# Kernel optimization log

Measured on AMD Instinct MI355X. Metric: run time of the kernel, lower is better.

Reference implementation:

```python
import jax, jax.numpy as jnp
import numpy as np

NIN = 1024
NOUT = 1024
NHEADS = 16
DHEAD = NOUT // NHEADS


def setup_inputs() -> dict:
    key = jax.random.key(0)
    k1, k2, k3, k4 = jax.random.split(key, 4)
    y = jax.random.normal(k1, (2, 2048, NIN), dtype=jnp.float32)
    Wqkv = jax.random.normal(k2, (NIN, 3 * NOUT), dtype=jnp.float32) * (1.0 / np.sqrt(NIN))
    Wff = jax.random.normal(k3, (NOUT, NOUT), dtype=jnp.float32) * (1.0 / np.sqrt(NOUT))
    bff = jax.random.normal(k4, (NOUT,), dtype=jnp.float32) * 0.01
    return {"y": y, "Wqkv": Wqkv, "Wff": Wff, "bff": bff}


def reference(y, Wqkv, Wff, bff):
    b, n, _ = y.shape
    qkv = y @ Wqkv  # [b, n, 3*nout]
    qkv = qkv.reshape(b, n, 3, NHEADS, DHEAD).transpose(2, 0, 3, 1, 4)
    q, k, v = qkv[0], qkv[1], qkv[2]  # each [b, h, n, d]
    att = jnp.einsum('bhqd,bhkd->bhqk', q, k)
    causal = jnp.triu(jnp.ones((n, n), dtype=bool), k=1)
    att = jnp.where(causal, -jnp.inf, att)
    att = jax.nn.softmax(att / jnp.sqrt(jnp.float32(DHEAD)), axis=-1)
    ctx = jnp.einsum('bhqk,bhkd->bhqd', att, v)
    ctx = ctx.transpose(0, 2, 1, 3).reshape(b, n, NOUT)
    return ctx @ Wff + bff
```

## Files before the change

kernel.cpp:

```cpp
#include <hip/hip_runtime.h>
#include <stdint.h>

#define NHEADS 16
#define DHEAD 64
#define SEQ 2048
#define BATCH 2
#define NINF 1024
#define NOUTF 1024
#define N3 3072
#define MTOT 4096

typedef unsigned short US;
typedef __attribute__((ext_vector_type(8))) short short8;
typedef __attribute__((ext_vector_type(4))) short short4v;
typedef __attribute__((ext_vector_type(4))) float f32x4;

__device__ inline US f2bf(float f) {
  union { float f; unsigned u; } v; v.f = f;
  unsigned r = v.u + 0x7fffu + ((v.u >> 16) & 1u);
  return (US)(r >> 16);
}

__device__ inline f32x4 mfma16(short8 a, short8 b, f32x4 c) {
  return __builtin_amdgcn_mfma_f32_16x16x32_bf16(a, b, c, 0, 0, 0);
}

__device__ inline f32x4 mfma16k16(short4v a, short4v b, f32x4 c) {
  return __builtin_amdgcn_mfma_f32_16x16x16bf16_1k(a, b, c, 0, 0, 0);
}

__device__ inline void async16(const US* g, US* l) {
  __builtin_amdgcn_global_load_lds(
      (const __attribute__((address_space(1))) unsigned int*)g,
      (__attribute__((address_space(3))) unsigned int*)l, 16, 0, 0);
}

__global__ void k_convert(const float* __restrict__ src, US* __restrict__ dst, int n4) {
  int i = blockIdx.x * blockDim.x + threadIdx.x;
  if (i >= n4) return;
  float4 v = ((const float4*)src)[i];
  ushort4 o;
  o.x = f2bf(v.x); o.y = f2bf(v.y); o.z = f2bf(v.z); o.w = f2bf(v.w);
  ((ushort4*)dst)[i] = o;
}

__global__ void k_wtrans(const float* __restrict__ Wqkv, const float* __restrict__ Wff,
                         US* __restrict__ dq, US* __restrict__ df) {
  __shared__ float tile[32][33];
  int bxi = blockIdx.x;
  const float* src; US* dst; int C;
  if (bxi < 96) { src = Wqkv; dst = dq; C = N3; }
  else          { src = Wff;  dst = df; C = NOUTF; bxi -= 96; }
  int bx = bxi * 32, by = blockIdx.y * 32;
  int tx = threadIdx.x, ty = threadIdx.y;
  for (int i = 0; i < 32; i += 8)
    tile[ty + i][tx] = src[(size_t)(by + ty + i) * C + bx + tx];
  __syncthreads();
  for (int i = 0; i < 32; i += 8)
    dst[(size_t)(bx + ty + i) * 1024 + by + tx] = f2bf(tile[tx][ty + i]);
}

__global__ void k_vtrans(const US* __restrict__ src, US* __restrict__ dst) {
  __shared__ US tile[32][33];
  int bh = blockIdx.z;
  int bx = blockIdx.x * 32;
  int by = blockIdx.y * 32;
  int tx = threadIdx.x, ty = threadIdx.y;
  const US* s0 = src + (size_t)bh * SEQ * DHEAD;
  US* d0 = dst + (size_t)bh * DHEAD * SEQ;
  for (int i = 0; i < 32; i += 8)
    tile[ty + i][tx] = s0[(size_t)(by + ty + i) * DHEAD + bx + tx];
  __syncthreads();
  for (int i = 0; i < 32; i += 8)
    d0[(size_t)(bx + ty + i) * SEQ + by + tx] = tile[tx][ty + i];
}

__global__ __launch_bounds__(256) void k_gemm_qkv(
    const US* __restrict__ A,
    const US* __restrict__ Bt,
    US* __restrict__ qbuf, US* __restrict__ kbuf, US* __restrict__ vbuf) {
  __shared__ US As[128 * 32];
  __shared__ US Bs[128 * 32];
  int tid = threadIdx.x;
  int wave = tid >> 6, lane = tid & 63, lm = lane & 15, lk = lane >> 4;
  int wm = wave >> 1, wn = wave & 1;
  int mbase = blockIdx.y * 128, nbase = blockIdx.x * 128;

  f32x4 acc[4][4];
#pragma unroll
  for (int i = 0; i < 4; ++i)
#pragma unroll
    for (int j = 0; j < 4; ++j) acc[i][j] = (f32x4){0.f, 0.f, 0.f, 0.f};

  const US* ga = A + (size_t)(mbase + (tid >> 2)) * NINF + (tid & 3) * 8;
  const US* gb = Bt + (size_t)(nbase + (tid >> 2)) * NINF + (tid & 3) * 8;
  US* la = As + tid * 8;
  US* lb = Bs + tid * 8;

  for (int kt = 0; kt < NINF / 32; ++kt) {
    int ko = kt * 32;
    async16(ga + ko, la);
    async16(ga + ko + (size_t)64 * NINF, la + 64 * 32);
    async16(gb + ko, lb);
    async16(gb + ko + (size_t)64 * NINF, lb + 64 * 32);
    __syncthreads();
    short8 a[4], b[4];
#pragma unroll
    for (int i = 0; i < 4; ++i)
      a[i] = *(const short8*)(As + (wm * 64 + i * 16 + lm) * 32 + lk * 8);
#pragma unroll
    for (int j = 0; j < 4; ++j)
      b[j] = *(const short8*)(Bs + (wn * 64 + j * 16 + lm) * 32 + lk * 8);
#pragma unroll
    for (int i = 0; i < 4; ++i)
#pragma unroll
      for (int j = 0; j < 4; ++j) acc[i][j] = mfma16(a[i], b[j], acc[i][j]);
    __syncthreads();
  }

  int which = nbase >> 10;
  US* dsts = (which == 0) ? qbuf : (which == 1) ? kbuf : vbuf;
  float sc = (which == 0) ? 0.18033688011112042f : 1.f;
#pragma unroll
  for (int j = 0; j < 4; ++j) {
    int col = nbase + wn * 64 + j * 16 + lm;
    int hh = (col & 1023) >> 6;
    int d = col & 63;
#pragma unroll
    for (int i = 0; i < 4; ++i) {
#pragma unroll
      for (int r = 0; r < 4; ++r) {
        int row = mbase + wm * 64 + i * 16 + lk * 4 + r;
        int bb = row >> 11;
        int s = row & (SEQ - 1);
        int bh = bb * NHEADS + hh;
        dsts[((size_t)bh * SEQ + s) * DHEAD + d] = f2bf(acc[i][j][r] * sc);
      }
    }
  }
}

__global__ __launch_bounds__(256) void k_attn(
    const US* __restrict__ qbuf, const US* __restrict__ kbuf,
    const US* __restrict__ vtbuf, US* __restrict__ ctx) {
  __shared__ US Ks[2][64 * 64];
  __shared__ US Vs[2][64 * 64];
  int tid = threadIdx.x;
  int w = tid >> 6, lane = tid & 63;
  int lm = lane & 15, lk = lane >> 4;
  int bl = blockIdx.x;
  int xcd = bl & 7, g = bl >> 3;
  int bh = (g & 3) * 8 + xcd;
  int q4 = g >> 2;
  int rr = q4 >> 3, qq = q4 & 7;
  int s = (rr == 0) ? 31 - qq : (rr == 1) ? qq : (rr == 2) ? 23 - qq : 8 + qq;
  int qb = s * 64 + w * 16;
  int nt = s + 1;

  const US* kbase = kbuf + (size_t)bh * SEQ * DHEAD;
  const US* vtb = vtbuf + (size_t)bh * DHEAD * SEQ;
  const US* qr = qbuf + ((size_t)bh * SEQ + qb + lm) * DHEAD + lk * 8;
  short8 qf0 = *(const short8*)(qr);
  short8 qf1 = *(const short8*)(qr + 32);

  int swz = ((lane & 7) ^ (lane >> 3)) * 8;
  const US* gsrc[4];
  US* ldst[4];
  int step[4];
#pragma unroll
  for (int j = 0; j < 4; ++j) {
    int u = w + 4 * j;
    if (u < 8) {
      gsrc[j] = kbase + (size_t)(u * 8 + (lane >> 3)) * DHEAD + swz;
      ldst[j] = &Ks[0][0] + u * 512 + lane * 8;
      step[j] = 64 * DHEAD;
    } else {
      int i = u - 8;
      gsrc[j] = vtb + (size_t)(i * 8 + (lane >> 3)) * SEQ + swz;
      ldst[j] = &Vs[0][0] + i * 512 + lane * 8;
      step[j] = 64;
    }
  }

  int xorv = lm & 7;
  int ck0 = ((lk) ^ xorv) * 16;
  int ck1 = ((4 + lk) ^ xorv) * 16;
  int cv[4];
#pragma unroll
  for (int kg = 0; kg < 4; ++kg)
    cv[kg] = (((kg * 2 + (lk >> 1)) ^ xorv) * 16) + (lk & 1) * 8;

  f32x4 o[4];
#pragma unroll
  for (int dg = 0; dg < 4; ++dg) o[dg] = (f32x4){0.f, 0.f, 0.f, 0.f};
  f32x4 lacc = (f32x4){0.f, 0.f, 0.f, 0.f};
  const short4v kones = {(short)0x3F80, (short)0x3F80, (short)0x3F80, (short)0x3F80};

  auto body = [&](const char* Kc, const char* Vc, int kg, bool dm) {
    const char* kr = Kc + (kg * 16 + lm) * 128;
    short8 ka0 = *(const short8*)(kr + ck0);
    short8 ka1 = *(const short8*)(kr + ck1);
    f32x4 st = (f32x4){0.f, 0.f, 0.f, 0.f};
    st = mfma16(ka0, qf0, st);
    st = mfma16(ka1, qf1, st);
    uint32_t ue[4];
#pragma unroll
    for (int r = 0; r < 4; ++r) {
      float v = st[r];
      if (dm && (lk * 4 + r > lm)) v = -INFINITY;
      union { float f; uint32_t u; } cv2;
      cv2.f = exp2f(v);
      ue[r] = cv2.u + 0x8000u;
    }
    union { short4v s4; uint32_t u[2]; } pk;
    pk.u[0] = __builtin_amdgcn_perm(ue[1], ue[0], 0x07060302u);
    pk.u[1] = __builtin_amdgcn_perm(ue[3], ue[2], 0x07060302u);
    lacc = mfma16k16(kones, pk.s4, lacc);
    const char* vr = Vc + lm * 128 + cv[kg];
#pragma unroll
    for (int dg = 0; dg < 4; ++dg) {
      short4v va = *(const short4v*)(vr + dg * 2048);
      o[dg] = mfma16k16(va, pk.s4, o[dg]);
    }
  };

#pragma unroll
  for (int j = 0; j < 4; ++j) { async16(gsrc[j], ldst[j]); gsrc[j] += step[j]; }
  if (nt > 1) {
#pragma unroll
    for (int j = 0; j < 4; ++j) { async16(gsrc[j], ldst[j] + 4096); gsrc[j] += step[j]; }
  }

  for (int t = 0; t < nt; ++t) {
    if (t + 1 < nt) asm volatile("s_waitcnt vmcnt(4)" ::: "memory");
    else            asm volatile("s_waitcnt vmcnt(0)" ::: "memory");
    __builtin_amdgcn_s_barrier();
    asm volatile("" ::: "memory");
    const char* Kc = (const char*)Ks + (t & 1) * 8192;
    const char* Vc = (const char*)Vs + (t & 1) * 8192;
    if (t < s) {
#pragma unroll
      for (int kg = 0; kg < 4; ++kg) body(Kc, Vc, kg, false);
    } else {
      for (int kg = 0; kg < w; ++kg) body(Kc, Vc, kg, false);
      body(Kc, Vc, w, true);
    }
    asm volatile("" ::: "memory");
    __builtin_amdgcn_s_barrier();
    asm volatile("" ::: "memory");
    if (t + 2 < nt) {
#pragma unroll
      for (int j = 0; j < 4; ++j) {
        async16(gsrc[j], ldst[j] + (t & 1) * 4096);
        gsrc[j] += step[j];
      }
    }
  }

  float inv = 1.f / lacc[0];

  US* crow = ctx + ((size_t)(bh >> 4) * SEQ + qb + lm) * NOUTF + (bh & 15) * DHEAD;
#pragma unroll
  for (int dg = 0; dg < 4; ++dg) {
    union { short4v s4; uint32_t u[2]; } pk;
    pk.u[0] = (uint32_t)f2bf(o[dg][0] * inv) | ((uint32_t)f2bf(o[dg][1] * inv) << 16);
    pk.u[1] = (uint32_t)f2bf(o[dg][2] * inv) | ((uint32_t)f2bf(o[dg][3] * inv) << 16);
    *(short4v*)(crow + dg * 16 + lk * 4) = pk.s4;
  }
}

__global__ __launch_bounds__(256) void k_gemm_out(
    const US* __restrict__ A, const US* __restrict__ Bt,
    const float* __restrict__ bias, float* __restrict__ out) {
  __shared__ US As[128 * 32];
  __shared__ US Bs[64 * 32];
  int tid = threadIdx.x;
  int wave = tid >> 6, lane = tid & 63, lm = lane & 15, lk = lane >> 4;
  int mbase = blockIdx.y * 128, nbase = blockIdx.x * 64;

  f32x4 acc[2][4];
#pragma unroll
  for (int i = 0; i < 2; ++i)
#pragma unroll
    for (int j = 0; j < 4; ++j) acc[i][j] = (f32x4){0.f, 0.f, 0.f, 0.f};

  const US* ga = A + (size_t)(mbase + (tid >> 2)) * NOUTF + (tid & 3) * 8;
  const US* gb = Bt + (size_t)(nbase + (tid >> 2)) * NOUTF + (tid & 3) * 8;
  US* la = As + tid * 8;
  US* lb = Bs + tid * 8;

  for (int kt = 0; kt < NOUTF / 32; ++kt) {
    int ko = kt * 32;
    async16(ga + ko, la);
    async16(ga + ko + (size_t)64 * NOUTF, la + 64 * 32);
    async16(gb + ko, lb);
    __syncthreads();
    short8 a[2], b[4];
#pragma unroll
    for (int i = 0; i < 2; ++i)
      a[i] = *(const short8*)(As + (wave * 32 + i * 16 + lm) * 32 + lk * 8);
#pragma unroll
    for (int j = 0; j < 4; ++j)
      b[j] = *(const short8*)(Bs + (j * 16 + lm) * 32 + lk * 8);
#pragma unroll
    for (int i = 0; i < 2; ++i)
#pragma unroll
      for (int j = 0; j < 4; ++j) acc[i][j] = mfma16(a[i], b[j], acc[i][j]);
    __syncthreads();
  }

#pragma unroll
  for (int j = 0; j < 4; ++j) {
    int col = nbase + j * 16 + lm;
    float bv = bias[col];
#pragma unroll
    for (int i = 0; i < 2; ++i)
#pragma unroll
      for (int r = 0; r < 4; ++r) {
        int row = mbase + wave * 32 + i * 16 + lk * 4 + r;
        out[(size_t)row * NOUTF + col] = acc[i][j][r] + bv;
      }
  }
}

extern "C" void kernel_launch(void* const* d_in, const int* in_sizes, int n_in,
                              void* d_out, int out_size, void* d_ws, size_t ws_size,
                              hipStream_t stream) {
  const float* y    = (const float*)d_in[0];
  const float* Wqkv = (const float*)d_in[1];
  const float* Wff  = (const float*)d_in[2];
  const float* bff  = (const float*)d_in[3];
  float* out = (float*)d_out;

  char* ws = (char*)d_ws;
  US* ybf   = (US*)(ws);
  US* ctx   = (US*)(ws);
  US* wqkvt = (US*)(ws + (8u << 20));
  US* wfft  = (US*)(ws + (14u << 20));
  US* qbuf  = (US*)(ws + (16u << 20));
  US* kbuf  = (US*)(ws + (24u << 20));
  US* vbuf  = (US*)(ws + (32u << 20));
  US* vtbuf = (US*)(ws + (40u << 20));

  k_convert<<<MTOT * NINF / 4 / 256, 256, 0, stream>>>(y, ybf, MTOT * NINF / 4);
  k_wtrans<<<dim3(128, 32), dim3(32, 8), 0, stream>>>(Wqkv, Wff, wqkvt, wfft);
  k_gemm_qkv<<<dim3(N3 / 128, MTOT / 128), 256, 0, stream>>>(ybf, wqkvt, qbuf, kbuf, vbuf);
  k_vtrans<<<dim3(DHEAD / 32, SEQ / 32, BATCH * NHEADS), dim3(32, 8), 0, stream>>>(vbuf, vtbuf);
  k_attn<<<dim3(1024), 256, 0, stream>>>(qbuf, kbuf, vtbuf, ctx);
  k_gemm_out<<<dim3(NOUTF / 64, MTOT / 128), 256, 0, stream>>>(ctx, wfft, bff, out);
}
```

Measured before the change: 184.1 us.

## Merge preprocessing kernels, vectorize GEMM epilogues via swapped MFMA operands, retile output GEMM

Fuses the y conversion and weight transpose into one launch, saving a kernel launch. In the QKV and output GEMMs, the MFMA operands are swapped so each lane holds four consecutive columns. That lets the epilogues write packed 8-byte bf16 and 16-byte float4 stores instead of scattered scalar stores. The output GEMM tile shrinks to 64x64 with a 2x2 wave layout, doubling the block count for better occupancy on 256 CUs, at the cost of less reuse per block.

```diff
diff --git a/kernel.cpp b/kernel.cpp
--- a/kernel.cpp
+++ b/kernel.cpp
@@ -35,29 +35,33 @@
       (__attribute__((address_space(3))) unsigned int*)l, 16, 0, 0);
 }
 
-__global__ void k_convert(const float* __restrict__ src, US* __restrict__ dst, int n4) {
-  int i = blockIdx.x * blockDim.x + threadIdx.x;
-  if (i >= n4) return;
-  float4 v = ((const float4*)src)[i];
-  ushort4 o;
-  o.x = f2bf(v.x); o.y = f2bf(v.y); o.z = f2bf(v.z); o.w = f2bf(v.w);
-  ((ushort4*)dst)[i] = o;
-}
-
-__global__ void k_wtrans(const float* __restrict__ Wqkv, const float* __restrict__ Wff,
-                         US* __restrict__ dq, US* __restrict__ df) {
+__global__ __launch_bounds__(256) void k_pre(
+    const float* __restrict__ y, US* __restrict__ ybf,
+    const float* __restrict__ Wqkv, const float* __restrict__ Wff,
+    US* __restrict__ dq, US* __restrict__ df) {
   __shared__ float tile[32][33];
-  int bxi = blockIdx.x;
-  const float* src; US* dst; int C;
-  if (bxi < 96) { src = Wqkv; dst = dq; C = N3; }
-  else          { src = Wff;  dst = df; C = NOUTF; bxi -= 96; }
-  int bx = bxi * 32, by = blockIdx.y * 32;
-  int tx = threadIdx.x, ty = threadIdx.y;
-  for (int i = 0; i < 32; i += 8)
-    tile[ty + i][tx] = src[(size_t)(by + ty + i) * C + bx + tx];
-  __syncthreads();
-  for (int i = 0; i < 32; i += 8)
-    dst[(size_t)(bx + ty + i) * 1024 + by + tx] = f2bf(tile[tx][ty + i]);
+  int bl = blockIdx.x;
+  int tid = threadIdx.x;
+  if (bl < 4096) {
+    int i = bl * 256 + tid;
+    float4 v = ((const float4*)y)[i];
+    ushort4 o;
+    o.x = f2bf(v.x); o.y = f2bf(v.y); o.z = f2bf(v.z); o.w = f2bf(v.w);
+    ((ushort4*)ybf)[i] = o;
+  } else {
+    int bl2 = bl - 4096;
+    int bxi = bl2 & 127, byi = bl2 >> 7;
+    const float* src; US* dst; int C;
+    if (bxi < 96) { src = Wqkv; dst = dq; C = N3; }
+    else          { src = Wff;  dst = df; C = NOUTF; bxi -= 96; }
+    int bx = bxi * 32, by = byi * 32;
+    int tx = tid & 31, ty = tid >> 5;
+    for (int i = 0; i < 32; i += 8)
+      tile[ty + i][tx] = src[(size_t)(by + ty + i) * C + bx + tx];
+    __syncthreads();
+    for (int i = 0; i < 32; i += 8)
+      dst[(size_t)(bx + ty + i) * 1024 + by + tx] = f2bf(tile[tx][ty + i]);
+  }
 }
 
 __global__ void k_vtrans(const US* __restrict__ src, US* __restrict__ dst) {
@@ -114,28 +118,27 @@
 #pragma unroll
     for (int i = 0; i < 4; ++i)
 #pragma unroll
-      for (int j = 0; j < 4; ++j) acc[i][j] = mfma16(a[i], b[j], acc[i][j]);
+      for (int j = 0; j < 4; ++j) acc[i][j] = mfma16(b[j], a[i], acc[i][j]);
     __syncthreads();
   }
 
   int which = nbase >> 10;
   US* dsts = (which == 0) ? qbuf : (which == 1) ? kbuf : vbuf;
   float sc = (which == 0) ? 0.18033688011112042f : 1.f;
-#pragma unroll
-  for (int j = 0; j < 4; ++j) {
-    int col = nbase + wn * 64 + j * 16 + lm;
-    int hh = (col & 1023) >> 6;
-    int d = col & 63;
-#pragma unroll
-    for (int i = 0; i < 4; ++i) {
-#pragma unroll
-      for (int r = 0; r < 4; ++r) {
-        int row = mbase + wm * 64 + i * 16 + lk * 4 + r;
-        int bb = row >> 11;
-        int s = row & (SEQ - 1);
-        int bh = bb * NHEADS + hh;
-        dsts[((size_t)bh * SEQ + s) * DHEAD + d] = f2bf(acc[i][j][r] * sc);
-      }
+  int hh = ((nbase + wn * 64) & 1023) >> 6;
+#pragma unroll
+  for (int i = 0; i < 4; ++i) {
+    int row = mbase + wm * 64 + i * 16 + lm;
+    int bh = (row >> 11) * NHEADS + hh;
+    int s = row & (SEQ - 1);
+    US* base = dsts + ((size_t)bh * SEQ + s) * DHEAD;
+#pragma unroll
+    for (int j = 0; j < 4; ++j) {
+      int d0 = j * 16 + lk * 4;
+      uint32_t lo = (uint32_t)f2bf(acc[i][j][0] * sc) | ((uint32_t)f2bf(acc[i][j][1] * sc) << 16);
+      uint32_t hi = (uint32_t)f2bf(acc[i][j][2] * sc) | ((uint32_t)f2bf(acc[i][j][3] * sc) << 16);
+      uint2 pv; pv.x = lo; pv.y = hi;
+      *(uint2*)(base + d0) = pv;
     }
   }
 }
@@ -152,8 +155,8 @@
   int xcd = bl & 7, g = bl >> 3;
   int bh = (g & 3) * 8 + xcd;
   int q4 = g >> 2;
-  int rr = q4 >> 3, qq = q4 & 7;
-  int s = (rr == 0) ? 31 - qq : (rr == 1) ? qq : (rr == 2) ? 23 - qq : 8 + qq;
+  int rnd = q4 >> 3, qq = q4 & 7;
+  int s = (rnd == 0) ? 31 - qq : (rnd == 1) ? qq : (rnd == 2) ? 23 - qq : 8 + qq;
   int qb = s * 64 + w * 16;
   int nt = s + 1;
 
@@ -272,17 +275,18 @@
 __global__ __launch_bounds__(256) void k_gemm_out(
     const US* __restrict__ A, const US* __restrict__ Bt,
     const float* __restrict__ bias, float* __restrict__ out) {
-  __shared__ US As[128 * 32];
+  __shared__ US As[64 * 32];
   __shared__ US Bs[64 * 32];
   int tid = threadIdx.x;
   int wave = tid >> 6, lane = tid & 63, lm = lane & 15, lk = lane >> 4;
-  int mbase = blockIdx.y * 128, nbase = blockIdx.x * 64;
-
-  f32x4 acc[2][4];
+  int wm = wave >> 1, wn = wave & 1;
+  int mbase = blockIdx.y * 64, nbase = blockIdx.x * 64;
+
+  f32x4 acc[2][2];
 #pragma unroll
   for (int i = 0; i < 2; ++i)
 #pragma unroll
-    for (int j = 0; j < 4; ++j) acc[i][j] = (f32x4){0.f, 0.f, 0.f, 0.f};
+    for (int j = 0; j < 2; ++j) acc[i][j] = (f32x4){0.f, 0.f, 0.f, 0.f};
 
   const US* ga = A + (size_t)(mbase + (tid >> 2)) * NOUTF + (tid & 3) * 8;
   const US* gb = Bt + (size_t)(nbase + (tid >> 2)) * NOUTF + (tid & 3) * 8;
@@ -292,34 +296,36 @@
   for (int kt = 0; kt < NOUTF / 32; ++kt) {
     int ko = kt * 32;
     async16(ga + ko, la);
-    async16(ga + ko + (size_t)64 * NOUTF, la + 64 * 32);
     async16(gb + ko, lb);
     __syncthreads();
-    short8 a[2], b[4];
+    short8 a[2], b[2];
 #pragma unroll
     for (int i = 0; i < 2; ++i)
-      a[i] = *(const short8*)(As + (wave * 32 + i * 16 + lm) * 32 + lk * 8);
-#pragma unroll
-    for (int j = 0; j < 4; ++j)
-      b[j] = *(const short8*)(Bs + (j * 16 + lm) * 32 + lk * 8);
+      a[i] = *(const short8*)(As + (wm * 32 + i * 16 + lm) * 32 + lk * 8);
+#pragma unroll
+    for (int j = 0; j < 2; ++j)
+      b[j] = *(const short8*)(Bs + (wn * 32 + j * 16 + lm) * 32 + lk * 8);
 #pragma unroll
     for (int i = 0; i < 2; ++i)
 #pragma unroll
-      for (int j = 0; j < 4; ++j) acc[i][j] = mfma16(a[i], b[j], acc[i][j]);
-    __syncthreads();
-  }
-
-#pragma unroll
-  for (int j = 0; j < 4; ++j) {
-    int col = nbase + j * 16 + lm;
-    float bv = bias[col];
-#pragma unroll
-    for (int i = 0; i < 2; ++i)
-#pragma unroll
-      for (int r = 0; r < 4; ++r) {
-        int row = mbase + wave * 32 + i * 16 + lk * 4 + r;
-        out[(size_t)row * NOUTF + col] = acc[i][j][r] + bv;
-      }
+      for (int j = 0; j < 2; ++j) acc[i][j] = mfma16(b[j], a[i], acc[i][j]);
+    __syncthreads();
+  }
+
+#pragma unroll
+  for (int j = 0; j < 2; ++j) {
+    int n0 = nbase + wn * 32 + j * 16 + lk * 4;
+    float4 bv = *(const float4*)(bias + n0);
+#pragma unroll
+    for (int i = 0; i < 2; ++i) {
+      int row = mbase + wm * 32 + i * 16 + lm;
+      float4 ov;
+      ov.x = acc[i][j][0] + bv.x;
+      ov.y = acc[i][j][1] + bv.y;
+      ov.z = acc[i][j][2] + bv.z;
+      ov.w = acc[i][j][3] + bv.w;
+      *(float4*)(out + (size_t)row * NOUTF + n0) = ov;
+    }
   }
 }
 
@@ -342,10 +348,9 @@
   US* vbuf  = (US*)(ws + (32u << 20));
   US* vtbuf = (US*)(ws + (40u << 20));
 
-  k_convert<<<MTOT * NINF / 4 / 256, 256, 0, stream>>>(y, ybf, MTOT * NINF / 4);
-  k_wtrans<<<dim3(128, 32), dim3(32, 8), 0, stream>>>(Wqkv, Wff, wqkvt, wfft);
+  k_pre<<<dim3(8192), 256, 0, stream>>>(y, ybf, Wqkv, Wff, wqkvt, wfft);
   k_gemm_qkv<<<dim3(N3 / 128, MTOT / 128), 256, 0, stream>>>(ybf, wqkvt, qbuf, kbuf, vbuf);
   k_vtrans<<<dim3(DHEAD / 32, SEQ / 32, BATCH * NHEADS), dim3(32, 8), 0, stream>>>(vbuf, vtbuf);
   k_attn<<<dim3(1024), 256, 0, stream>>>(qbuf, kbuf, vtbuf, ctx);
-  k_gemm_out<<<dim3(NOUTF / 64, MTOT / 128), 256, 0, stream>>>(ctx, wfft, bff, out);
-}
+  k_gemm_out<<<dim3(NOUTF / 64, MTOT / 64), 256, 0, stream>>>(ctx, wfft, bff, out);
+}
```

Result: no change. 183.0 us (-0.6%).
